# Performance work log

Measured on AMD Instinct MI355X. Metric: run time of the kernel, lower is better.

## Reference

```python
import jax, jax.numpy as jnp
import numpy as np

V, E, S_MAX, H, L = 32000, 1024, 2048, 16, 6
D = E // H  # head_dim = 64
EPS = 1e-5


def _ln(x, g, b):
    mu = jnp.mean(x, axis=-1, keepdims=True)
    var = jnp.mean(jnp.square(x - mu), axis=-1, keepdims=True)
    return (x - mu) * jax.lax.rsqrt(var + EPS) * g + b


def setup_inputs() -> dict:
    key = jax.random.key(0)
    ks = iter(jax.random.split(key, 32))
    std = 0.02
    B, S = 1, 2048
    inp = {
        "tokens": jax.random.randint(next(ks), (B, S), 0, V, dtype=jnp.int32),
        "W_emb": jax.random.normal(next(ks), (V, E), jnp.float32) * std,  # tied with fc_out
        "W_pos": jax.random.normal(next(ks), (S_MAX, E), jnp.float32) * std,
        # per-layer stacked params [L, ...]
        "Wq": jax.random.normal(next(ks), (L, E, E), jnp.float32) * std,
        "Wk": jax.random.normal(next(ks), (L, E, E), jnp.float32) * std,
        "Wv": jax.random.normal(next(ks), (L, E, E), jnp.float32) * std,
        "Wo": jax.random.normal(next(ks), (L, E, E), jnp.float32) * std,
        "bo": jnp.zeros((L, E), jnp.float32),
        "ln1_g": jnp.ones((L, E), jnp.float32),
        "ln1_b": jnp.zeros((L, E), jnp.float32),
        "ln2_g": jnp.ones((L, E), jnp.float32),
        "ln2_b": jnp.zeros((L, E), jnp.float32),
        "W1": jax.random.normal(next(ks), (L, 4 * E, E), jnp.float32) * std,
        "b1": jnp.zeros((L, 4 * E), jnp.float32),
        "W2": jax.random.normal(next(ks), (L, E, 4 * E), jnp.float32) * std,
        "b2": jnp.zeros((L, E), jnp.float32),
        "lnf_g": jnp.ones((E,), jnp.float32),
        "lnf_b": jnp.zeros((E,), jnp.float32),
    }
    return inp


def _gpt_forward(tokens, W_emb, W_pos, Wq, Wk, Wv, Wo, bo, ln1_g, ln1_b,
                 ln2_g, ln2_b, W1, b1, W2, b2, lnf_g, lnf_b):
    B, S = tokens.shape
    x = W_emb[tokens] + W_pos[:S][None, :, :]  # [B,S,E]
    causal = jnp.tril(jnp.ones((S, S), bool))  # [S,S]
    scale = 1.0 / np.sqrt(D)

    def block(x, p):
        wq, wk, wv, wo, bo_, g1, b1n, g2, b2n, w1, bf1, w2, bf2 = p
        h = _ln(x, g1, b1n)
        # torch Linear: y = x @ W.T ; split heads -> [B,H,S,D]
        def heads(w):
            return (h @ w.T).reshape(B, S, H, D).transpose(0, 2, 1, 3)
        q, k, v = heads(wq), heads(wk), heads(wv)
        scores = jnp.einsum('bhqd,bhkd->bhqk', q, k) * scale
        scores = jnp.where(causal[None, None], scores, -jnp.inf)
        attn = jax.nn.softmax(scores, axis=-1)
        o = jnp.einsum('bhqk,bhkd->bhqd', attn, v)
        o = o.transpose(0, 2, 1, 3).reshape(B, S, E)
        x = x + o @ wo.T + bo_
        h2 = _ln(x, g2, b2n)
        ff = jax.nn.gelu(h2 @ w1.T + bf1, approximate=False) @ w2.T + bf2
        return x + ff, None

    params = (Wq, Wk, Wv, Wo, bo, ln1_g, ln1_b, ln2_g, ln2_b, W1, b1, W2, b2)
    x, _ = jax.lax.scan(block, x, params)
    x = _ln(x, lnf_g, lnf_b)
    return x @ W_emb.T  # tied output projection [B,S,V]


def reference(tokens, W_emb, W_pos, Wq, Wk, Wv, Wo, bo, ln1_g, ln1_b,
              ln2_g, ln2_b, W1, b1, W2, b2, lnf_g, lnf_b):
    return _gpt_forward(tokens, W_emb, W_pos, Wq, Wk, Wv, Wo, bo, ln1_g,
                        ln1_b, ln2_g, ln2_b, W1, b1, W2, b2, lnf_g, lnf_b)
```

## Files before the change

### kernel.cpp

```cpp
#include <hip/hip_runtime.h>
#include <math.h>

#define S_LEN 2048
#define EMB 1024
#define NHEAD 16
#define HDIM 64
#define NLAYER 6
#define VOCAB 32000
#define FFDIM 4096

using f32x4 = __attribute__((ext_vector_type(4))) float;
using bf16x8 = __attribute__((ext_vector_type(8))) __bf16;
typedef unsigned short us;

static __device__ __forceinline__ unsigned short f2bf(float f) {
  union { float f; unsigned int u; } v; v.f = f;
  unsigned int r = v.u + 0x7FFFu + ((v.u >> 16) & 1u);
  return (unsigned short)(r >> 16);
}

#define GLOAD_LDS16(g, l)                                                      \
  __builtin_amdgcn_global_load_lds(                                            \
      (const __attribute__((address_space(1))) void*)(g),                      \
      (__attribute__((address_space(3))) void*)(l), 16, 0, 0)

__global__ __launch_bounds__(256) void cvt_bf16_kernel(
    const float* __restrict__ in, us* __restrict__ out, long n) {
  long i = ((long)blockIdx.x * 256 + threadIdx.x) * 8;
  if (i >= n) return;
  const float4* p = (const float4*)(in + i);
  float4 a = p[0], b = p[1];
  uint4 o;
  o.x = (unsigned)f2bf(a.x) | ((unsigned)f2bf(a.y) << 16);
  o.y = (unsigned)f2bf(a.z) | ((unsigned)f2bf(a.w) << 16);
  o.z = (unsigned)f2bf(b.x) | ((unsigned)f2bf(b.y) << 16);
  o.w = (unsigned)f2bf(b.z) | ((unsigned)f2bf(b.w) << 16);
  *(uint4*)(out + i) = o;
}

__global__ __launch_bounds__(256) void embed_kernel(
    const int* __restrict__ tok, const float* __restrict__ Wemb,
    const float* __restrict__ Wpos, float* __restrict__ x) {
  int s = blockIdx.x, t = threadIdx.x;
  int tk = tok[s];
  const float4* we = (const float4*)(Wemb + (size_t)tk * EMB);
  const float4* wp = (const float4*)(Wpos + (size_t)s * EMB);
  float4 a = we[t], b = wp[t];
  float4 o; o.x = a.x + b.x; o.y = a.y + b.y; o.z = a.z + b.z; o.w = a.w + b.w;
  ((float4*)(x + (size_t)s * EMB))[t] = o;
}

__global__ __launch_bounds__(256) void ln_kernel(
    const float* __restrict__ x, const float* __restrict__ g,
    const float* __restrict__ b, us* __restrict__ out) {
  int row = blockIdx.x, t = threadIdx.x, lane = t & 63, wave = t >> 6;
  float4 v = ((const float4*)(x + (size_t)row * EMB))[t];
  float s = v.x + v.y + v.z + v.w;
  float q = v.x * v.x + v.y * v.y + v.z * v.z + v.w * v.w;
  #pragma unroll
  for (int d = 1; d < 64; d <<= 1) { s += __shfl_xor(s, d); q += __shfl_xor(q, d); }
  __shared__ float rs[4], rq[4];
  if (lane == 0) { rs[wave] = s; rq[wave] = q; }
  __syncthreads();
  s = rs[0] + rs[1] + rs[2] + rs[3];
  q = rq[0] + rq[1] + rq[2] + rq[3];
  float mean = s * (1.0f / EMB);
  float var = q * (1.0f / EMB) - mean * mean;
  float rstd = rsqrtf(var + 1e-5f);
  float4 gg = ((const float4*)g)[t], bb = ((const float4*)b)[t];
  ushort4 o;
  o.x = f2bf((v.x - mean) * rstd * gg.x + bb.x);
  o.y = f2bf((v.y - mean) * rstd * gg.y + bb.y);
  o.z = f2bf((v.z - mean) * rstd * gg.z + bb.z);
  o.w = f2bf((v.w - mean) * rstd * gg.w + bb.w);
  ((ushort4*)(out + (size_t)row * EMB))[t] = o;
}

template <int SK>
__global__ __launch_bounds__(256) void reduce_ln_kernel(
    float* __restrict__ x, const float* __restrict__ p,
    const float* __restrict__ bias, const float* __restrict__ g,
    const float* __restrict__ b, us* __restrict__ out) {
  int row = blockIdx.x, t = threadIdx.x, lane = t & 63, wave = t >> 6;
  const size_t plane = (size_t)S_LEN * EMB;
  float4 v = ((const float4*)(x + (size_t)row * EMB))[t];
  float4 bb4 = ((const float4*)bias)[t];
  v.x += bb4.x; v.y += bb4.y; v.z += bb4.z; v.w += bb4.w;
  #pragma unroll
  for (int z = 0; z < SK; ++z) {
    float4 q4 = ((const float4*)(p + z * plane + (size_t)row * EMB))[t];
    v.x += q4.x; v.y += q4.y; v.z += q4.z; v.w += q4.w;
  }
  ((float4*)(x + (size_t)row * EMB))[t] = v;
  float s = v.x + v.y + v.z + v.w;
  float q = v.x * v.x + v.y * v.y + v.z * v.z + v.w * v.w;
  #pragma unroll
  for (int d = 1; d < 64; d <<= 1) { s += __shfl_xor(s, d); q += __shfl_xor(q, d); }
  __shared__ float rs[4], rq[4];
  if (lane == 0) { rs[wave] = s; rq[wave] = q; }
  __syncthreads();
  s = rs[0] + rs[1] + rs[2] + rs[3];
  q = rq[0] + rq[1] + rq[2] + rq[3];
  float mean = s * (1.0f / EMB);
  float var = q * (1.0f / EMB) - mean * mean;
  float rstd = rsqrtf(var + 1e-5f);
  float4 gg = ((const float4*)g)[t], lb = ((const float4*)b)[t];
  ushort4 o;
  o.x = f2bf((v.x - mean) * rstd * gg.x + lb.x);
  o.y = f2bf((v.y - mean) * rstd * gg.y + lb.y);
  o.z = f2bf((v.z - mean) * rstd * gg.z + lb.z);
  o.w = f2bf((v.w - mean) * rstd * gg.w + lb.w);
  ((ushort4*)(out + (size_t)row * EMB))[t] = o;
}

template <int HAS_BIAS, int HAS_RES, int DO_GELU, int OUT_BF16>
__global__ __launch_bounds__(256) void gemm_bb(
    const us* __restrict__ A, const us* __restrict__ B0,
    const us* __restrict__ B1, const us* __restrict__ B2,
    const float* __restrict__ bias, const float* __restrict__ res,
    void* C0, void* C1, void* C2, int M, int N, int K) {
  const us* B = blockIdx.z == 0 ? B0 : (blockIdx.z == 1 ? B1 : B2);
  void* C = blockIdx.z == 0 ? C0 : (blockIdx.z == 1 ? C1 : C2);
  const int nwg = gridDim.x * gridDim.y;
  int lin = blockIdx.y * gridDim.x + blockIdx.x;
  {
    const int qx = nwg >> 3, r = nwg & 7;
    const int xcd = lin & 7, idx = lin >> 3;
    lin = (xcd < r ? xcd * (qx + 1) : r * (qx + 1) + (xcd - r) * qx) + idx;
  }
  const int m0 = (lin % gridDim.x) * 128, n0 = (lin / gridDim.x) * 128;
  const int t = threadIdx.x, lane = t & 63, wave = t >> 6;
  const int wm = (wave >> 1) * 64, wn = (wave & 1) * 64;
  __shared__ __align__(16) us As[128 * 64];
  __shared__ __align__(16) us Bs[128 * 64];
  f32x4 acc[4][4] = {};
  const int kIters = K >> 6;
  const int cbase = wave * 64;
  const int myc = cbase + lane;
  for (int kt = 0; kt < kIters; ++kt) {
    const int k0 = kt << 6;
    __syncthreads();
    #pragma unroll
    for (int i = 0; i < 4; ++i) {
      const int c = myc + i * 256;
      const int row = c >> 3, col = (c & 7) * 8;
      GLOAD_LDS16(A + (size_t)(m0 + row) * K + k0 + col,
                  As + (size_t)(cbase + i * 256) * 8);
    }
    #pragma unroll
    for (int i = 0; i < 4; ++i) {
      const int c = myc + i * 256;
      const int row = c >> 3, col = (c & 7) * 8;
      GLOAD_LDS16(B + (size_t)(n0 + row) * K + k0 + col,
                  Bs + (size_t)(cbase + i * 256) * 8);
    }
    __syncthreads();
    #pragma unroll
    for (int ks = 0; ks < 2; ++ks) {
      bf16x8 af[4], bfr[4];
      #pragma unroll
      for (int i = 0; i < 4; ++i)
        af[i] = *(const bf16x8*)(As + (wm + i * 16 + (lane & 15)) * 64 + ks * 32 + (lane >> 4) * 8);
      #pragma unroll
      for (int j = 0; j < 4; ++j)
        bfr[j] = *(const bf16x8*)(Bs + (wn + j * 16 + (lane & 15)) * 64 + ks * 32 + (lane >> 4) * 8);
      #pragma unroll
      for (int i = 0; i < 4; ++i)
        #pragma unroll
        for (int j = 0; j < 4; ++j)
          acc[i][j] = __builtin_amdgcn_mfma_f32_16x16x32_bf16(af[i], bfr[j], acc[i][j], 0, 0, 0);
    }
  }
  const int r0 = (lane >> 4) * 4, cl = lane & 15;
  #pragma unroll
  for (int i = 0; i < 4; ++i) {
    #pragma unroll
    for (int j = 0; j < 4; ++j) {
      const int col = n0 + wn + j * 16 + cl;
      float bv = HAS_BIAS ? bias[col] : 0.0f;
      #pragma unroll
      for (int r = 0; r < 4; ++r) {
        const int row = m0 + wm + i * 16 + r0 + r;
        float val = acc[i][j][r] + bv;
        if (DO_GELU) val = val * 0.5f * (1.0f + erff(val * 0.70710678118f));
        if (HAS_RES) val += res[(size_t)row * N + col];
        if (OUT_BF16) ((us*)C)[(size_t)row * N + col] = f2bf(val);
        else          ((float*)C)[(size_t)row * N + col] = val;
      }
    }
  }
}

__global__ __launch_bounds__(256) void gemm_sk(
    const us* __restrict__ A, const us* __restrict__ B,
    float* __restrict__ C, int M, int N, int K, int kSlice) {
  const int z = blockIdx.z;
  const int nwg = gridDim.x * gridDim.y;
  int lin = blockIdx.y * gridDim.x + blockIdx.x;
  {
    const int qx = nwg >> 3, r = nwg & 7;
    const int xcd = lin & 7, idx = lin >> 3;
    lin = (xcd < r ? xcd * (qx + 1) : r * (qx + 1) + (xcd - r) * qx) + idx;
  }
  const int m0 = (lin % gridDim.x) * 128, n0 = (lin / gridDim.x) * 128;
  const int t = threadIdx.x, lane = t & 63, wave = t >> 6;
  const int wm = (wave >> 1) * 64, wn = (wave & 1) * 64;
  __shared__ __align__(16) us As[128 * 64];
  __shared__ __align__(16) us Bs[128 * 64];
  f32x4 acc[4][4] = {};
  const int cbase = wave * 64;
  const int myc = cbase + lane;
  const int kBeg = z * kSlice;
  const int kIters = kSlice >> 6;
  for (int kt = 0; kt < kIters; ++kt) {
    const int k0 = kBeg + (kt << 6);
    __syncthreads();
    #pragma unroll
    for (int i = 0; i < 4; ++i) {
      const int c = myc + i * 256;
      const int row = c >> 3, col = (c & 7) * 8;
      GLOAD_LDS16(A + (size_t)(m0 + row) * K + k0 + col,
                  As + (size_t)(cbase + i * 256) * 8);
    }
    #pragma unroll
    for (int i = 0; i < 4; ++i) {
      const int c = myc + i * 256;
      const int row = c >> 3, col = (c & 7) * 8;
      GLOAD_LDS16(B + (size_t)(n0 + row) * K + k0 + col,
                  Bs + (size_t)(cbase + i * 256) * 8);
    }
    __syncthreads();
    #pragma unroll
    for (int ks = 0; ks < 2; ++ks) {
      bf16x8 af[4], bfr[4];
      #pragma unroll
      for (int i = 0; i < 4; ++i)
        af[i] = *(const bf16x8*)(As + (wm + i * 16 + (lane & 15)) * 64 + ks * 32 + (lane >> 4) * 8);
      #pragma unroll
      for (int j = 0; j < 4; ++j)
        bfr[j] = *(const bf16x8*)(Bs + (wn + j * 16 + (lane & 15)) * 64 + ks * 32 + (lane >> 4) * 8);
      #pragma unroll
      for (int i = 0; i < 4; ++i)
        #pragma unroll
        for (int j = 0; j < 4; ++j)
          acc[i][j] = __builtin_amdgcn_mfma_f32_16x16x32_bf16(af[i], bfr[j], acc[i][j], 0, 0, 0);
    }
  }
  float* Cz = C + (size_t)z * M * N;
  const int r0 = (lane >> 4) * 4, cl = lane & 15;
  #pragma unroll
  for (int i = 0; i < 4; ++i)
    #pragma unroll
    for (int j = 0; j < 4; ++j) {
      const int col = n0 + wn + j * 16 + cl;
      #pragma unroll
      for (int r = 0; r < 4; ++r)
        Cz[(size_t)(m0 + wm + i * 16 + r0 + r) * N + col] = acc[i][j][r];
    }
}

__global__ __launch_bounds__(512, 1) void gemm_v8p(
    const us* __restrict__ A, const us* __restrict__ B,
    float* __restrict__ C, int M, int N, int K) {
  const int nwg = gridDim.x * gridDim.y;
  int lin = blockIdx.y * gridDim.x + blockIdx.x;
  {
    const int qx = nwg >> 3, r = nwg & 7;
    const int xcd = lin & 7, idx = lin >> 3;
    lin = (xcd < r ? xcd * (qx + 1) : r * (qx + 1) + (xcd - r) * qx) + idx;
  }
  const int m0 = (lin % gridDim.x) * 256, n0 = (lin / gridDim.x) * 256;
  const int t = threadIdx.x, lane = t & 63, wave = t >> 6;
  const int lq = lane & 15, hi = lane >> 4;
  const int rbase = (wave >> 2) * 128, cbase = (wave & 3) * 64;
  __shared__ __align__(16) us As[3][256 * 32];
  __shared__ __align__(16) us Bs[3][256 * 32];
  f32x4 acc[8][4] = {};
  const int nt = K >> 5;

#define STAGE_T(MAT, LDSB, TT)                                                 \
  {                                                                            \
    const int kk0 = (TT) << 5;                                                 \
    _Pragma("unroll")                                                          \
    for (int i_ = 0; i_ < 2; ++i_) {                                           \
      const int ci = t + i_ * 512;                                             \
      const int rr = ci >> 2, cc = ci & 3;                                     \
      const int src = (cc ^ ((rr >> 1) & 3)) * 8;                              \
      GLOAD_LDS16(MAT + (size_t)(((MAT == A) ? m0 : n0) + rr) * K + kk0 + src, \
                  &LDSB[0] + (wave * 64 + i_ * 512) * 8);                      \
    }                                                                          \
  }

  STAGE_T(A, As[0], 0); STAGE_T(B, Bs[0], 0);
  STAGE_T(A, As[1], 1); STAGE_T(B, Bs[1], 1);
  STAGE_T(A, As[2], 2); STAGE_T(B, Bs[2], 2);
  asm volatile("s_waitcnt vmcnt(8)" ::: "memory");
  __builtin_amdgcn_s_barrier();
  __builtin_amdgcn_sched_barrier(0);

  int bb = 0;
  for (int tt = 0; tt < nt; ++tt) {
    const int sb = (bb + 2 >= 3) ? bb - 1 : bb + 2;
    const us* Ab = &As[bb][0];
    const us* Bb = &Bs[bb][0];
    bf16x8 a0[4], a1[4], b0[4];
    #pragma unroll
    for (int f = 0; f < 4; ++f) {
      const int row = rbase + f * 16 + lq;
      a0[f] = *(const bf16x8*)(Ab + row * 32 + ((hi ^ ((row >> 1) & 3)) * 8));
    }
    #pragma unroll
    for (int f = 0; f < 4; ++f) {
      const int row = rbase + 64 + f * 16 + lq;
      a1[f] = *(const bf16x8*)(Ab + row * 32 + ((hi ^ ((row >> 1) & 3)) * 8));
    }
    #pragma unroll
    for (int f = 0; f < 4; ++f) {
      const int row = cbase + f * 16 + lq;
      b0[f] = *(const bf16x8*)(Bb + row * 32 + ((hi ^ ((row >> 1) & 3)) * 8));
    }
    if (tt + 2 < nt) {
      STAGE_T(A, As[sb], tt + 2);
      STAGE_T(B, Bs[sb], tt + 2);
    }
    __builtin_amdgcn_s_setprio(1);
    #pragma unroll
    for (int i = 0; i < 4; ++i)
      #pragma unroll
      for (int j = 0; j < 4; ++j)
        acc[i][j] = __builtin_amdgcn_mfma_f32_16x16x32_bf16(a0[i], b0[j], acc[i][j], 0, 0, 0);
    #pragma unroll
    for (int i = 0; i < 4; ++i)
      #pragma unroll
      for (int j = 0; j < 4; ++j)
        acc[4 + i][j] = __builtin_amdgcn_mfma_f32_16x16x32_bf16(a1[i], b0[j], acc[4 + i][j], 0, 0, 0);
    __builtin_amdgcn_s_setprio(0);
    if (tt + 2 < nt) {
      asm volatile("s_waitcnt vmcnt(4)" ::: "memory");
    } else {
      asm volatile("s_waitcnt vmcnt(0)" ::: "memory");
    }
    __builtin_amdgcn_s_barrier();
    __builtin_amdgcn_sched_barrier(0);
    bb = (bb + 1 == 3) ? 0 : bb + 1;
  }
#undef STAGE_T
  #pragma unroll
  for (int i = 0; i < 8; ++i)
    #pragma unroll
    for (int j = 0; j < 4; ++j) {
      const int col = n0 + cbase + j * 16 + lq;
      #pragma unroll
      for (int r = 0; r < 4; ++r)
        C[(size_t)(m0 + rbase + i * 16 + hi * 4 + r) * N + col] = acc[i][j][r];
    }
}

__global__ __launch_bounds__(256) void attn_kernel(
    const us* __restrict__ qb, const us* __restrict__ kb,
    const us* __restrict__ vb, us* __restrict__ ob) {
  const int qt = gridDim.x - 1 - blockIdx.x;
  const int head = blockIdx.y;
  const int t = threadIdx.x, lane = t & 63, wave = t >> 6;
  const int hi = lane >> 4, lq = lane & 15;
  const int hd = head * HDIM;
  const int q0w = qt * 64 + wave * 16;
  __shared__ __align__(16) us Kl[2][64 * 64];
  __shared__ __align__(16) us Vl[2][64 * 72];
  __shared__ __align__(16) us Pl[4][16][72];
  bf16x8 qf[2];
  {
    const us* qp = qb + (size_t)(q0w + lq) * EMB + hd + hi * 8;
    qf[0] = *(const bf16x8*)qp;
    qf[1] = *(const bf16x8*)(qp + 32);
    #pragma unroll
    for (int e = 0; e < 8; ++e) {
      qf[0][e] = (__bf16)((float)qf[0][e] * 0.125f);
      qf[1][e] = (__bf16)((float)qf[1][e] * 0.125f);
    }
  }
  f32x4 accO[4] = {};
  float m_run = -1e30f, l_run = 0.f;
  const int vr2 = (t >> 3) * 2, d8 = (t & 7) * 8;
  const int q_g = q0w + lq;

  {
    #pragma unroll
    for (int i = 0; i < 2; ++i) {
      const int c = wave * 64 + lane + i * 256;
      const int row = c >> 3, j = c & 7;
      const int colE = (j * 8) ^ ((row & 7) << 3);
      GLOAD_LDS16(kb + (size_t)(row) * EMB + hd + colE,
                  &Kl[0][0] + (wave * 64 + i * 256) * 8);
    }
    const us* vp = vb + (size_t)vr2 * EMB + hd + d8;
    uint4 vA = *(const uint4*)vp;
    uint4 vB = *(const uint4*)(vp + EMB);
    const unsigned* wa = (const unsigned*)&vA;
    const unsigned* wb = (const unsigned*)&vB;
    #pragma unroll
    for (int i = 0; i < 8; ++i) {
      unsigned lo = (i & 1) ? (wa[i >> 1] >> 16) : (wa[i >> 1] & 0xffffu);
      unsigned hw = (i & 1) ? (wb[i >> 1] >> 16) : (wb[i >> 1] & 0xffffu);
      *(unsigned*)(&Vl[0][0] + (d8 + i) * 72 + vr2) = lo | (hw << 16);
    }
  }
  __syncthreads();
  int cur = 0;
  for (int kt = 0; kt <= qt; ++kt) {
    uint4 vA, vB;
    if (kt < qt) {
      #pragma unroll
      for (int i = 0; i < 2; ++i) {
        const int c = wave * 64 + lane + i * 256;
        const int row = c >> 3, j = c & 7;
        const int colE = (j * 8) ^ ((row & 7) << 3);
        GLOAD_LDS16(kb + (size_t)((kt + 1) * 64 + row) * EMB + hd + colE,
                    &Kl[cur ^ 1][0] + (wave * 64 + i * 256) * 8);
      }
      const us* vp = vb + (size_t)((kt + 1) * 64 + vr2) * EMB + hd + d8;
      vA = *(const uint4*)vp;
      vB = *(const uint4*)(vp + EMB);
    }
    f32x4 sc[4] = {};
    #pragma unroll
    for (int ks = 0; ks < 2; ++ks) {
      #pragma unroll
      for (int fn = 0; fn < 4; ++fn) {
        const int rowk = fn * 16 + lq;
        const us* kp = &Kl[cur][0] + rowk * 64 + ((ks * 32 + hi * 8) ^ ((rowk & 7) << 3));
        sc[fn] = __builtin_amdgcn_mfma_f32_16x16x32_bf16(
            *(const bf16x8*)kp, qf[ks], sc[fn], 0, 0, 0);
      }
    }
    float pv[16];
    float pmax = -1e30f;
    if (kt == qt) {
      #pragma unroll
      for (int fn = 0; fn < 4; ++fn)
        #pragma unroll
        for (int r = 0; r < 4; ++r) {
          const int k_g = kt * 64 + fn * 16 + hi * 4 + r;
          float sv = sc[fn][r];
          if (k_g > q_g) sv = -1e30f;
          pv[fn * 4 + r] = sv;
          pmax = fmaxf(pmax, sv);
        }
    } else {
      #pragma unroll
      for (int fn = 0; fn < 4; ++fn)
        #pragma unroll
        for (int r = 0; r < 4; ++r) {
          float sv = sc[fn][r];
          pv[fn * 4 + r] = sv;
          pmax = fmaxf(pmax, sv);
        }
    }
    pmax = fmaxf(pmax, __shfl_xor(pmax, 16));
    pmax = fmaxf(pmax, __shfl_xor(pmax, 32));
    if (!__all(pmax <= m_run + 8.0f)) {
      const float mn = fmaxf(m_run, pmax);
      const float alpha = __expf(m_run - mn);
      m_run = mn;
      l_run *= alpha;
      float ar[4];
      #pragma unroll
      for (int r = 0; r < 4; ++r) ar[r] = __shfl(alpha, hi * 4 + r);
      #pragma unroll
      for (int df = 0; df < 4; ++df)
        #pragma unroll
        for (int r = 0; r < 4; ++r) accO[df][r] *= ar[r];
    }
    float rsum = 0.f;
    #pragma unroll
    for (int i = 0; i < 16; ++i) {
      float e = __expf(pv[i] - m_run);
      pv[i] = e;
      rsum += e;
    }
    rsum += __shfl_xor(rsum, 16);
    rsum += __shfl_xor(rsum, 32);
    l_run += rsum;
    #pragma unroll
    for (int fn = 0; fn < 4; ++fn) {
      ushort4 pk;
      pk.x = f2bf(pv[fn * 4 + 0]);
      pk.y = f2bf(pv[fn * 4 + 1]);
      pk.z = f2bf(pv[fn * 4 + 2]);
      pk.w = f2bf(pv[fn * 4 + 3]);
      *(ushort4*)&Pl[wave][lq][fn * 16 + hi * 4] = pk;
    }
    #pragma unroll
    for (int ks = 0; ks < 2; ++ks) {
      bf16x8 pf = *(const bf16x8*)&Pl[wave][lq][ks * 32 + hi * 8];
      #pragma unroll
      for (int df = 0; df < 4; ++df) {
        bf16x8 vf = *(const bf16x8*)(&Vl[cur][0] + (df * 16 + lq) * 72 + ks * 32 + hi * 8);
        accO[df] = __builtin_amdgcn_mfma_f32_16x16x32_bf16(pf, vf, accO[df], 0, 0, 0);
      }
    }
    if (kt < qt) {
      const unsigned* wa = (const unsigned*)&vA;
      const unsigned* wb = (const unsigned*)&vB;
      #pragma unroll
      for (int i = 0; i < 8; ++i) {
        unsigned lo = (i & 1) ? (wa[i >> 1] >> 16) : (wa[i >> 1] & 0xffffu);
        unsigned hw = (i & 1) ? (wb[i >> 1] >> 16) : (wb[i >> 1] & 0xffffu);
        *(unsigned*)(&Vl[cur ^ 1][0] + (d8 + i) * 72 + vr2) = lo | (hw << 16);
      }
    }
    __syncthreads();
    cur ^= 1;
  }
  float linv[4];
  #pragma unroll
  for (int r = 0; r < 4; ++r) linv[r] = 1.0f / __shfl(l_run, hi * 4 + r);
  #pragma unroll
  for (int r = 0; r < 4; ++r) {
    const int row = q0w + hi * 4 + r;
    #pragma unroll
    for (int df = 0; df < 4; ++df)
      ob[(size_t)row * EMB + hd + df * 16 + lq] = f2bf(accO[df][r] * linv[r]);
  }
}

extern "C" void kernel_launch(void* const* d_in, const int* in_sizes, int n_in,
                              void* d_out, int out_size, void* d_ws, size_t ws_size,
                              hipStream_t stream) {
  const int* tok = (const int*)d_in[0];
  const float* Wemb = (const float*)d_in[1];
  const float* Wpos = (const float*)d_in[2];
  const float* Wq = (const float*)d_in[3];
  const float* Wk = (const float*)d_in[4];
  const float* Wv = (const float*)d_in[5];
  const float* Wo = (const float*)d_in[6];
  const float* bo = (const float*)d_in[7];
  const float* ln1g = (const float*)d_in[8];
  const float* ln1b = (const float*)d_in[9];
  const float* ln2g = (const float*)d_in[10];
  const float* ln2b = (const float*)d_in[11];
  const float* W1 = (const float*)d_in[12];
  const float* b1 = (const float*)d_in[13];
  const float* W2 = (const float*)d_in[14];
  const float* b2 = (const float*)d_in[15];
  const float* lnfg = (const float*)d_in[16];
  const float* lnfb = (const float*)d_in[17];
  (void)in_sizes; (void)n_in; (void)out_size;

  const size_t MB = 1u << 20;
  char* ws = (char*)d_ws;
  float* x = (float*)ws;
  us* h  = (us*)(ws + 8 * MB);
  us* qb = (us*)(ws + 12 * MB);
  us* kb = (us*)(ws + 16 * MB);
  us* vb = (us*)(ws + 20 * MB);
  us* ob = (us*)(ws + 24 * MB);
  us* fb = (us*)(ws + 12 * MB);
  us* cWq = (us*)(ws + 28 * MB);
  us* cWk = (us*)(ws + 40 * MB);
  us* cWv = (us*)(ws + 52 * MB);
  us* cWo = (us*)(ws + 64 * MB);
  us* cW1 = (us*)(ws + 76 * MB);
  us* cW2 = (us*)(ws + 124 * MB);
  us* cWemb = (us*)(ws + 172 * MB);
  float* pbuf = (float*)(ws + 236 * MB);
  const size_t need_bf16 = 172 * MB + (size_t)VOCAB * EMB * 2;
  const bool bf16w = ws_size >= need_bf16;
  int skWo = 0, skF2 = 0;
  if (ws_size >= 236 * MB + 32 * MB)      { skWo = 2; skF2 = 4; }
  else if (ws_size >= 236 * MB + 16 * MB) { skWo = 2; skF2 = 2; }
  const bool fused = (skWo == 2 && skF2 == 4);

  embed_kernel<<<dim3(S_LEN), 256, 0, stream>>>(tok, Wemb, Wpos, x);
  if (!bf16w) return;

  const long nE2 = (long)NLAYER * EMB * EMB;
  const long nF  = (long)NLAYER * FFDIM * EMB;
  const long nV  = (long)VOCAB * EMB;
  cvt_bf16_kernel<<<(int)(nE2 / 2048), 256, 0, stream>>>(Wq, cWq, nE2);
  cvt_bf16_kernel<<<(int)(nE2 / 2048), 256, 0, stream>>>(Wk, cWk, nE2);
  cvt_bf16_kernel<<<(int)(nE2 / 2048), 256, 0, stream>>>(Wv, cWv, nE2);
  cvt_bf16_kernel<<<(int)(nE2 / 2048), 256, 0, stream>>>(Wo, cWo, nE2);
  cvt_bf16_kernel<<<(int)(nF / 2048), 256, 0, stream>>>(W1, cW1, nF);
  cvt_bf16_kernel<<<(int)(nF / 2048), 256, 0, stream>>>(W2, cW2, nF);
  cvt_bf16_kernel<<<(int)(nV / 2048), 256, 0, stream>>>(Wemb, cWemb, nV);

  ln_kernel<<<S_LEN, 256, 0, stream>>>(x, ln1g, ln1b, h);
  for (int l = 0; l < NLAYER; ++l) {
    const size_t wofs = (size_t)l * EMB * EMB;
    const size_t fofs = (size_t)l * FFDIM * EMB;
    gemm_bb<0, 0, 0, 1><<<dim3(16, 8, 3), 256, 0, stream>>>(
        h, cWq + wofs, cWk + wofs, cWv + wofs, nullptr, nullptr,
        qb, kb, vb, S_LEN, EMB, EMB);
    attn_kernel<<<dim3(32, NHEAD), 256, 0, stream>>>(qb, kb, vb, ob);
    if (fused) {
      gemm_sk<<<dim3(16, 8, 2), 256, 0, stream>>>(
          ob, cWo + wofs, pbuf, S_LEN, EMB, EMB, EMB / 2);
      reduce_ln_kernel<2><<<S_LEN, 256, 0, stream>>>(
          x, pbuf, bo + l * EMB, ln2g + l * EMB, ln2b + l * EMB, h);
      gemm_bb<1, 0, 1, 1><<<dim3(16, 32, 1), 256, 0, stream>>>(
          h, cW1 + fofs, nullptr, nullptr, b1 + l * FFDIM, nullptr,
          fb, nullptr, nullptr, S_LEN, FFDIM, EMB);
      gemm_sk<<<dim3(16, 8, 4), 256, 0, stream>>>(
          fb, cW2 + fofs, pbuf, S_LEN, EMB, FFDIM, FFDIM / 4);
      if (l < NLAYER - 1)
        reduce_ln_kernel<4><<<S_LEN, 256, 0, stream>>>(
            x, pbuf, b2 + l * EMB, ln1g + (l + 1) * EMB, ln1b + (l + 1) * EMB, h);
      else
        reduce_ln_kernel<4><<<S_LEN, 256, 0, stream>>>(
            x, pbuf, b2 + l * EMB, lnfg, lnfb, h);
    } else {
      gemm_bb<1, 1, 0, 0><<<dim3(16, 8, 1), 256, 0, stream>>>(
          ob, cWo + wofs, nullptr, nullptr, bo + l * EMB, x,
          x, nullptr, nullptr, S_LEN, EMB, EMB);
      ln_kernel<<<S_LEN, 256, 0, stream>>>(x, ln2g + l * EMB, ln2b + l * EMB, h);
      gemm_bb<1, 0, 1, 1><<<dim3(16, 32, 1), 256, 0, stream>>>(
          h, cW1 + fofs, nullptr, nullptr, b1 + l * FFDIM, nullptr,
          fb, nullptr, nullptr, S_LEN, FFDIM, EMB);
      gemm_bb<1, 1, 0, 0><<<dim3(16, 8, 1), 256, 0, stream>>>(
          fb, cW2 + fofs, nullptr, nullptr, b2 + l * EMB, x,
          x, nullptr, nullptr, S_LEN, EMB, FFDIM);
      if (l < NLAYER - 1)
        ln_kernel<<<S_LEN, 256, 0, stream>>>(x, ln1g + (l + 1) * EMB, ln1b + (l + 1) * EMB, h);
      else
        ln_kernel<<<S_LEN, 256, 0, stream>>>(x, lnfg, lnfb, h);
    }
  }
  gemm_v8p<<<dim3(8, 125), 512, 0, stream>>>(
      h, cWemb, (float*)d_out, S_LEN, VOCAB, EMB);
}
```

Before: 1.460 ms.

## Triple-buffer GEMM K-loop with async LDS loads and XOR-swizzled tiles

```diff
diff --git a/kernel.cpp b/kernel.cpp
--- a/kernel.cpp
+++ b/kernel.cpp
@@ -113,11 +113,24 @@
   ((ushort4*)(out + (size_t)row * EMB))[t] = o;
 }
 
-template <int HAS_BIAS, int HAS_RES, int DO_GELU, int OUT_BF16>
-__global__ __launch_bounds__(256) void gemm_bb(
+#define STAGE_R(MATP, BROW, LDSB, TT)                                          \
+  {                                                                            \
+    const int kk0 = (TT) << 5;                                                 \
+    _Pragma("unroll")                                                          \
+    for (int i_ = 0; i_ < 2; ++i_) {                                           \
+      const int ci = t + i_ * 256;                                             \
+      const int rr = ci >> 2, cc = ci & 3;                                     \
+      const int src = (cc ^ ((rr >> 1) & 3)) * 8;                              \
+      GLOAD_LDS16(MATP + (size_t)((BROW) + rr) * K + kk0 + src,                \
+                  &LDSB[0] + (wave * 64 + i_ * 256) * 8);                      \
+    }                                                                          \
+  }
+
+template <int HAS_BIAS, int DO_GELU, int OUT_BF16>
+__global__ __launch_bounds__(256) void gemm_r128(
     const us* __restrict__ A, const us* __restrict__ B0,
     const us* __restrict__ B1, const us* __restrict__ B2,
-    const float* __restrict__ bias, const float* __restrict__ res,
+    const float* __restrict__ bias,
     void* C0, void* C1, void* C2, int M, int N, int K) {
   const us* B = blockIdx.z == 0 ? B0 : (blockIdx.z == 1 ? B1 : B2);
   void* C = blockIdx.z == 0 ? C0 : (blockIdx.z == 1 ? C1 : C2);
@@ -130,60 +143,68 @@
   }
   const int m0 = (lin % gridDim.x) * 128, n0 = (lin / gridDim.x) * 128;
   const int t = threadIdx.x, lane = t & 63, wave = t >> 6;
+  const int lq = lane & 15, hi = lane >> 4;
   const int wm = (wave >> 1) * 64, wn = (wave & 1) * 64;
-  __shared__ __align__(16) us As[128 * 64];
-  __shared__ __align__(16) us Bs[128 * 64];
+  __shared__ __align__(16) us As[3][128 * 32];
+  __shared__ __align__(16) us Bs[3][128 * 32];
   f32x4 acc[4][4] = {};
-  const int kIters = K >> 6;
-  const int cbase = wave * 64;
-  const int myc = cbase + lane;
-  for (int kt = 0; kt < kIters; ++kt) {
-    const int k0 = kt << 6;
-    __syncthreads();
-    #pragma unroll
-    for (int i = 0; i < 4; ++i) {
-      const int c = myc + i * 256;
-      const int row = c >> 3, col = (c & 7) * 8;
-      GLOAD_LDS16(A + (size_t)(m0 + row) * K + k0 + col,
-                  As + (size_t)(cbase + i * 256) * 8);
-    }
-    #pragma unroll
-    for (int i = 0; i < 4; ++i) {
-      const int c = myc + i * 256;
-      const int row = c >> 3, col = (c & 7) * 8;
-      GLOAD_LDS16(B + (size_t)(n0 + row) * K + k0 + col,
-                  Bs + (size_t)(cbase + i * 256) * 8);
-    }
-    __syncthreads();
-    #pragma unroll
-    for (int ks = 0; ks < 2; ++ks) {
-      bf16x8 af[4], bfr[4];
-      #pragma unroll
-      for (int i = 0; i < 4; ++i)
-        af[i] = *(const bf16x8*)(As + (wm + i * 16 + (lane & 15)) * 64 + ks * 32 + (lane >> 4) * 8);
+  const int nt = K >> 5;
+
+  STAGE_R(A, m0, As[0], 0); STAGE_R(B, n0, Bs[0], 0);
+  STAGE_R(A, m0, As[1], 1); STAGE_R(B, n0, Bs[1], 1);
+  STAGE_R(A, m0, As[2], 2); STAGE_R(B, n0, Bs[2], 2);
+  asm volatile("s_waitcnt vmcnt(8)" ::: "memory");
+  __builtin_amdgcn_s_barrier();
+  __builtin_amdgcn_sched_barrier(0);
+
+  int bb = 0;
+  for (int tt = 0; tt < nt; ++tt) {
+    const int sb = (bb + 2 >= 3) ? bb - 1 : bb + 2;
+    const us* Ab = &As[bb][0];
+    const us* Bb = &Bs[bb][0];
+    bf16x8 a[4], b[4];
+    #pragma unroll
+    for (int f = 0; f < 4; ++f) {
+      const int row = wm + f * 16 + lq;
+      a[f] = *(const bf16x8*)(Ab + row * 32 + ((hi ^ ((row >> 1) & 3)) * 8));
+    }
+    #pragma unroll
+    for (int f = 0; f < 4; ++f) {
+      const int row = wn + f * 16 + lq;
+      b[f] = *(const bf16x8*)(Bb + row * 32 + ((hi ^ ((row >> 1) & 3)) * 8));
+    }
+    if (tt + 2 < nt) {
+      STAGE_R(A, m0, As[sb], tt + 2);
+      STAGE_R(B, n0, Bs[sb], tt + 2);
+    }
+    __builtin_amdgcn_s_setprio(1);
+    #pragma unroll
+    for (int i = 0; i < 4; ++i)
       #pragma unroll
       for (int j = 0; j < 4; ++j)
-        bfr[j] = *(const bf16x8*)(Bs + (wn + j * 16 + (lane & 15)) * 64 + ks * 32 + (lane >> 4) * 8);
-      #pragma unroll
-      for (int i = 0; i < 4; ++i)
-        #pragma unroll
-        for (int j = 0; j < 4; ++j)
-          acc[i][j] = __builtin_amdgcn_mfma_f32_16x16x32_bf16(af[i], bfr[j], acc[i][j], 0, 0, 0);
-    }
-  }
-  const int r0 = (lane >> 4) * 4, cl = lane & 15;
+        acc[i][j] = __builtin_amdgcn_mfma_f32_16x16x32_bf16(a[i], b[j], acc[i][j], 0, 0, 0);
+    __builtin_amdgcn_s_setprio(0);
+    if (tt + 2 < nt) {
+      asm volatile("s_waitcnt vmcnt(4)" ::: "memory");
+    } else {
+      asm volatile("s_waitcnt vmcnt(0)" ::: "memory");
+    }
+    __builtin_amdgcn_s_barrier();
+    __builtin_amdgcn_sched_barrier(0);
+    bb = (bb + 1 == 3) ? 0 : bb + 1;
+  }
+  const int r0 = hi * 4;
   #pragma unroll
   for (int i = 0; i < 4; ++i) {
     #pragma unroll
     for (int j = 0; j < 4; ++j) {
-      const int col = n0 + wn + j * 16 + cl;
+      const int col = n0 + wn + j * 16 + lq;
       float bv = HAS_BIAS ? bias[col] : 0.0f;
       #pragma unroll
       for (int r = 0; r < 4; ++r) {
         const int row = m0 + wm + i * 16 + r0 + r;
         float val = acc[i][j][r] + bv;
         if (DO_GELU) val = val * 0.5f * (1.0f + erff(val * 0.70710678118f));
-        if (HAS_RES) val += res[(size_t)row * N + col];
         if (OUT_BF16) ((us*)C)[(size_t)row * N + col] = f2bf(val);
         else          ((float*)C)[(size_t)row * N + col] = val;
       }
@@ -191,7 +212,7 @@
   }
 }
 
-__global__ __launch_bounds__(256) void gemm_sk(
+__global__ __launch_bounds__(256) void gemm_rsk(
     const us* __restrict__ A, const us* __restrict__ B,
     float* __restrict__ C, int M, int N, int K, int kSlice) {
   const int z = blockIdx.z;
@@ -204,58 +225,66 @@
   }
   const int m0 = (lin % gridDim.x) * 128, n0 = (lin / gridDim.x) * 128;
   const int t = threadIdx.x, lane = t & 63, wave = t >> 6;
+  const int lq = lane & 15, hi = lane >> 4;
   const int wm = (wave >> 1) * 64, wn = (wave & 1) * 64;
-  __shared__ __align__(16) us As[128 * 64];
-  __shared__ __align__(16) us Bs[128 * 64];
+  __shared__ __align__(16) us As[3][128 * 32];
+  __shared__ __align__(16) us Bs[3][128 * 32];
   f32x4 acc[4][4] = {};
-  const int cbase = wave * 64;
-  const int myc = cbase + lane;
-  const int kBeg = z * kSlice;
-  const int kIters = kSlice >> 6;
-  for (int kt = 0; kt < kIters; ++kt) {
-    const int k0 = kBeg + (kt << 6);
-    __syncthreads();
-    #pragma unroll
-    for (int i = 0; i < 4; ++i) {
-      const int c = myc + i * 256;
-      const int row = c >> 3, col = (c & 7) * 8;
-      GLOAD_LDS16(A + (size_t)(m0 + row) * K + k0 + col,
-                  As + (size_t)(cbase + i * 256) * 8);
-    }
-    #pragma unroll
-    for (int i = 0; i < 4; ++i) {
-      const int c = myc + i * 256;
-      const int row = c >> 3, col = (c & 7) * 8;
-      GLOAD_LDS16(B + (size_t)(n0 + row) * K + k0 + col,
-                  Bs + (size_t)(cbase + i * 256) * 8);
-    }
-    __syncthreads();
-    #pragma unroll
-    for (int ks = 0; ks < 2; ++ks) {
-      bf16x8 af[4], bfr[4];
-      #pragma unroll
-      for (int i = 0; i < 4; ++i)
-        af[i] = *(const bf16x8*)(As + (wm + i * 16 + (lane & 15)) * 64 + ks * 32 + (lane >> 4) * 8);
+  const int nt = kSlice >> 5;
+  const int tb = z * (kSlice >> 5);
+
+  STAGE_R(A, m0, As[0], tb + 0); STAGE_R(B, n0, Bs[0], tb + 0);
+  STAGE_R(A, m0, As[1], tb + 1); STAGE_R(B, n0, Bs[1], tb + 1);
+  STAGE_R(A, m0, As[2], tb + 2); STAGE_R(B, n0, Bs[2], tb + 2);
+  asm volatile("s_waitcnt vmcnt(8)" ::: "memory");
+  __builtin_amdgcn_s_barrier();
+  __builtin_amdgcn_sched_barrier(0);
+
+  int bb = 0;
+  for (int tt = 0; tt < nt; ++tt) {
+    const int sb = (bb + 2 >= 3) ? bb - 1 : bb + 2;
+    const us* Ab = &As[bb][0];
+    const us* Bb = &Bs[bb][0];
+    bf16x8 a[4], b[4];
+    #pragma unroll
+    for (int f = 0; f < 4; ++f) {
+      const int row = wm + f * 16 + lq;
+      a[f] = *(const bf16x8*)(Ab + row * 32 + ((hi ^ ((row >> 1) & 3)) * 8));
+    }
+    #pragma unroll
+    for (int f = 0; f < 4; ++f) {
+      const int row = wn + f * 16 + lq;
+      b[f] = *(const bf16x8*)(Bb + row * 32 + ((hi ^ ((row >> 1) & 3)) * 8));
+    }
+    if (tt + 2 < nt) {
+      STAGE_R(A, m0, As[sb], tb + tt + 2);
+      STAGE_R(B, n0, Bs[sb], tb + tt + 2);
+    }
+    __builtin_amdgcn_s_setprio(1);
+    #pragma unroll
+    for (int i = 0; i < 4; ++i)
       #pragma unroll
       for (int j = 0; j < 4; ++j)
-        bfr[j] = *(const bf16x8*)(Bs + (wn + j * 16 + (lane & 15)) * 64 + ks * 32 + (lane >> 4) * 8);
-      #pragma unroll
-      for (int i = 0; i < 4; ++i)
-        #pragma unroll
-        for (int j = 0; j < 4; ++j)
-          acc[i][j] = __builtin_amdgcn_mfma_f32_16x16x32_bf16(af[i], bfr[j], acc[i][j], 0, 0, 0);
-    }
+        acc[i][j] = __builtin_amdgcn_mfma_f32_16x16x32_bf16(a[i], b[j], acc[i][j], 0, 0, 0);
+    __builtin_amdgcn_s_setprio(0);
+    if (tt + 2 < nt) {
+      asm volatile("s_waitcnt vmcnt(4)" ::: "memory");
+    } else {
+      asm volatile("s_waitcnt vmcnt(0)" ::: "memory");
+    }
+    __builtin_amdgcn_s_barrier();
+    __builtin_amdgcn_sched_barrier(0);
+    bb = (bb + 1 == 3) ? 0 : bb + 1;
   }
   float* Cz = C + (size_t)z * M * N;
-  const int r0 = (lane >> 4) * 4, cl = lane & 15;
   #pragma unroll
   for (int i = 0; i < 4; ++i)
     #pragma unroll
     for (int j = 0; j < 4; ++j) {
-      const int col = n0 + wn + j * 16 + cl;
+      const int col = n0 + wn + j * 16 + lq;
       #pragma unroll
       for (int r = 0; r < 4; ++r)
-        Cz[(size_t)(m0 + wm + i * 16 + r0 + r) * N + col] = acc[i][j][r];
+        Cz[(size_t)(m0 + wm + i * 16 + hi * 4 + r) * N + col] = acc[i][j][r];
     }
 }
 
@@ -564,15 +593,13 @@
   us* cW2 = (us*)(ws + 124 * MB);
   us* cWemb = (us*)(ws + 172 * MB);
   float* pbuf = (float*)(ws + 236 * MB);
-  const size_t need_bf16 = 172 * MB + (size_t)VOCAB * EMB * 2;
-  const bool bf16w = ws_size >= need_bf16;
-  int skWo = 0, skF2 = 0;
-  if (ws_size >= 236 * MB + 32 * MB)      { skWo = 2; skF2 = 4; }
-  else if (ws_size >= 236 * MB + 16 * MB) { skWo = 2; skF2 = 2; }
-  const bool fused = (skWo == 2 && skF2 == 4);
+  const size_t need = 236 * MB + 32 * MB;
+  if (ws_size < need) {
+    embed_kernel<<<dim3(S_LEN), 256, 0, stream>>>(tok, Wemb, Wpos, x);
+    return;
+  }
 
   embed_kernel<<<dim3(S_LEN), 256, 0, stream>>>(tok, Wemb, Wpos, x);
-  if (!bf16w) return;
 
   const long nE2 = (long)NLAYER * EMB * EMB;
   const long nF  = (long)NLAYER * FFDIM * EMB;
@@ -589,42 +616,25 @@
   for (int l = 0; l < NLAYER; ++l) {
     const size_t wofs = (size_t)l * EMB * EMB;
     const size_t fofs = (size_t)l * FFDIM * EMB;
-    gemm_bb<0, 0, 0, 1><<<dim3(16, 8, 3), 256, 0, stream>>>(
-        h, cWq + wofs, cWk + wofs, cWv + wofs, nullptr, nullptr,
+    gemm_r128<0, 0, 1><<<dim3(16, 8, 3), 256, 0, stream>>>(
+        h, cWq + wofs, cWk + wofs, cWv + wofs, nullptr,
         qb, kb, vb, S_LEN, EMB, EMB);
     attn_kernel<<<dim3(32, NHEAD), 256, 0, stream>>>(qb, kb, vb, ob);
-    if (fused) {
-      gemm_sk<<<dim3(16, 8, 2), 256, 0, stream>>>(
-          ob, cWo + wofs, pbuf, S_LEN, EMB, EMB, EMB / 2);
-      reduce_ln_kernel<2><<<S_LEN, 256, 0, stream>>>(
-          x, pbuf, bo + l * EMB, ln2g + l * EMB, ln2b + l * EMB, h);
-      gemm_bb<1, 0, 1, 1><<<dim3(16, 32, 1), 256, 0, stream>>>(
-          h, cW1 + fofs, nullptr, nullptr, b1 + l * FFDIM, nullptr,
-          fb, nullptr, nullptr, S_LEN, FFDIM, EMB);
-      gemm_sk<<<dim3(16, 8, 4), 256, 0, stream>>>(
-          fb, cW2 + fofs, pbuf, S_LEN, EMB, FFDIM, FFDIM / 4);
-      if (l < NLAYER - 1)
-        reduce_ln_kernel<4><<<S_LEN, 256, 0, stream>>>(
-            x, pbuf, b2 + l * EMB, ln1g + (l + 1) * EMB, ln1b + (l + 1) * EMB, h);
-      else
-        reduce_ln_kernel<4><<<S_LEN, 256, 0, stream>>>(
-            x, pbuf, b2 + l * EMB, lnfg, lnfb, h);
-    } else {
-      gemm_bb<1, 1, 0, 0><<<dim3(16, 8, 1), 256, 0, stream>>>(
-          ob, cWo + wofs, nullptr, nullptr, bo + l * EMB, x,
-          x, nullptr, nullptr, S_LEN, EMB, EMB);
-      ln_kernel<<<S_LEN, 256, 0, stream>>>(x, ln2g + l * EMB, ln2b + l * EMB, h);
-      gemm_bb<1, 0, 1, 1><<<dim3(16, 32, 1), 256, 0, stream>>>(
-          h, cW1 + fofs, nullptr, nullptr, b1 + l * FFDIM, nullptr,
-          fb, nullptr, nullptr, S_LEN, FFDIM, EMB);
-      gemm_bb<1, 1, 0, 0><<<dim3(16, 8, 1), 256, 0, stream>>>(
-          fb, cW2 + fofs, nullptr, nullptr, b2 + l * EMB, x,
-          x, nullptr, nullptr, S_LEN, EMB, FFDIM);
-      if (l < NLAYER - 1)
-        ln_kernel<<<S_LEN, 256, 0, stream>>>(x, ln1g + (l + 1) * EMB, ln1b + (l + 1) * EMB, h);
-      else
-        ln_kernel<<<S_LEN, 256, 0, stream>>>(x, lnfg, lnfb, h);
-    }
+    gemm_rsk<<<dim3(16, 8, 2), 256, 0, stream>>>(
+        ob, cWo + wofs, pbuf, S_LEN, EMB, EMB, EMB / 2);
+    reduce_ln_kernel<2><<<S_LEN, 256, 0, stream>>>(
+        x, pbuf, bo + l * EMB, ln2g + l * EMB, ln2b + l * EMB, h);
+    gemm_r128<1, 1, 1><<<dim3(16, 32, 1), 256, 0, stream>>>(
+        h, cW1 + fofs, nullptr, nullptr, b1 + l * FFDIM,
+        fb, nullptr, nullptr, S_LEN, FFDIM, EMB);
+    gemm_rsk<<<dim3(16, 8, 4), 256, 0, stream>>>(
+        fb, cW2 + fofs, pbuf, S_LEN, EMB, FFDIM, FFDIM / 4);
+    if (l < NLAYER - 1)
+      reduce_ln_kernel<4><<<S_LEN, 256, 0, stream>>>(
+          x, pbuf, b2 + l * EMB, ln1g + (l + 1) * EMB, ln1b + (l + 1) * EMB, h);
+    else
+      reduce_ln_kernel<4><<<S_LEN, 256, 0, stream>>>(
+          x, pbuf, b2 + l * EMB, lnfg, lnfb, h);
   }
   gemm_v8p<<<dim3(8, 125), 512, 0, stream>>>(
       h, cWemb, (float*)d_out, S_LEN, VOCAB, EMB);
```

Result: faster. 1.382 ms, median of 2 (-5.4%).
